# Kernel optimization log

Measured on AMD Instinct MI355X. Metric: run time of the kernel, lower is better.

## Reference

```python
import jax, jax.numpy as jnp
import numpy as np


def setup_inputs() -> dict:
    key = jax.random.key(0)
    k1, k2, k3, k4 = jax.random.split(key, 4)
    B, T, C, H = 256, 320, 1024, 64
    x = jax.random.normal(k1, (B, T, C), dtype=jnp.float32)
    # nn.Linear weights stored as (in, out) for x @ W
    scale = 1.0 / np.sqrt(C)
    W_key = jax.random.normal(k2, (C, H), dtype=jnp.float32) * scale
    W_query = jax.random.normal(k3, (C, H), dtype=jnp.float32) * scale
    W_value = jax.random.normal(k4, (C, H), dtype=jnp.float32) * scale
    return {"x": x, "W_key": W_key, "W_query": W_query, "W_value": W_value}


def reference(x, W_key, W_query, W_value):
    # Single-head causal self-attention. Dropout is identity (eval mode).
    B, T, C = x.shape
    k = x @ W_key     # [B,T,H]
    q = x @ W_query   # [B,T,H]
    v = x @ W_value   # [B,T,H]
    # NOTE: source scales by C**-0.5 with C = embd_size (input dim), not head_size.
    scale = jnp.asarray(C, x.dtype) ** -0.5
    wei = jnp.einsum("bth,bsh->bts", q, k) * scale  # [B,T,T]
    causal = jnp.tril(jnp.ones((T, T), dtype=bool))
    wei = jnp.where(causal, wei, -jnp.inf)
    wei = jax.nn.softmax(wei, axis=-1)
    out = jnp.einsum("bts,bsh->bth", wei, v)  # [B,T,H]
    return out
```

## Files before the change

kernel.cpp:

```cpp
#include <hip/hip_runtime.h>

typedef __bf16 bf16;
typedef __bf16 bf16x4 __attribute__((ext_vector_type(4)));
typedef __bf16 bf16x8 __attribute__((ext_vector_type(8)));
typedef float f32x4 __attribute__((ext_vector_type(4)));

#define MFMA16(a, b, c) __builtin_amdgcn_mfma_f32_16x16x32_bf16((a), (b), (c), 0, 0, 0)

#define GLD16(gp, lp)                                                              \
  __builtin_amdgcn_global_load_lds(                                                \
      (const __attribute__((address_space(1))) unsigned int*)(unsigned long long)(gp), \
      (__attribute__((address_space(3))) unsigned int*)(unsigned long long)(lp), 16, 0, 0)


__global__ __launch_bounds__(256) void wtrans_kernel(
    const float* __restrict__ Wk, const float* __restrict__ Wq,
    const float* __restrict__ Wv, bf16* __restrict__ Wt) {
  __shared__ bf16 tile[64][65];
  const int mat = blockIdx.x >> 4;
  const int kt = (blockIdx.x & 15) << 6;
  const float* __restrict__ W = (mat == 0) ? Wk : ((mat == 1) ? Wq : Wv);
  const int tid = threadIdx.x;
#pragma unroll
  for (int j = 0; j < 16; ++j) {
    const int i = tid + 256 * j;
    const int k = i >> 6, h = i & 63;
    tile[h][k] = (bf16)W[(kt + k) * 64 + h];
  }
  __syncthreads();
#pragma unroll
  for (int j = 0; j < 16; ++j) {
    const int i = tid + 256 * j;
    const int h = i >> 6, k = i & 63;
    Wt[mat * 65536 + h * 1024 + kt + k] = tile[h][k];
  }
}

__global__ __launch_bounds__(256) void qkv_kernel(
    const float* __restrict__ x, const bf16* __restrict__ Wt,
    bf16* __restrict__ Qw, bf16* __restrict__ Kw, bf16* __restrict__ Vt) {
  __shared__ float xs3[3][64][64];
  const int tid = threadIdx.x;
  const int w = tid >> 6, l = tid & 63;
  const int lr = l & 15, lg = l >> 4;
  const int m0 = blockIdx.x * 64;

  f32x4 acc[4][3];
#pragma unroll
  for (int mf = 0; mf < 4; ++mf)
#pragma unroll
    for (int nf = 0; nf < 3; ++nf) acc[mf][nf] = (f32x4)0.0f;

  const char* gb0;
  const char* gb1;
  const char* gb2;
  const char* gb3;
  {
    const int rr = l >> 4;
    const int cb = (l & 15) * 16;
    gb0 = (const char*)(x + (size_t)(m0 + 16 * w + 0 + rr) * 1024) + (cb ^ (((0 + rr) & 7) << 4));
    gb1 = (const char*)(x + (size_t)(m0 + 16 * w + 4 + rr) * 1024) + (cb ^ (((4 + rr) & 7) << 4));
    gb2 = (const char*)(x + (size_t)(m0 + 16 * w + 8 + rr) * 1024) + (cb ^ (((0 + rr) & 7) << 4));
    gb3 = (const char*)(x + (size_t)(m0 + 16 * w + 12 + rr) * 1024) + (cb ^ (((4 + rr) & 7) << 4));
  }

  bf16x8 wf[3][2];
  auto loadw = [&](int kt) {
#pragma unroll
    for (int nf = 0; nf < 3; ++nf) {
      const int colg = w * 48 + nf * 16 + lr;
      const bf16* p = Wt + (colg >> 6) * 65536 + (colg & 63) * 1024 + kt + lg * 8;
      wf[nf][0] = *(const bf16x8*)p;
      wf[nf][1] = *(const bf16x8*)(p + 32);
    }
  };
  auto dma = [&](int t) {
    char* lb = (char*)&xs3[t % 3][16 * w][0];
    const int ko = t * 256;
    GLD16(gb0 + ko, lb + 0 * 1024);
    GLD16(gb1 + ko, lb + 1 * 1024);
    GLD16(gb2 + ko, lb + 2 * 1024);
    GLD16(gb3 + ko, lb + 3 * 1024);
  };

  dma(0);
  dma(1);
  const int sw = (lr & 7) << 4;
#pragma unroll
  for (int t = 0; t < 16; ++t) {
    if (t < 15) {
      asm volatile("s_waitcnt vmcnt(4)" ::: "memory");
    } else {
      asm volatile("s_waitcnt vmcnt(0)" ::: "memory");
    }
    __builtin_amdgcn_sched_barrier(0);
    __builtin_amdgcn_s_barrier();
    __builtin_amdgcn_sched_barrier(0);
    loadw(t * 64);
    if (t < 14) dma(t + 2);
    const char* xb = (const char*)&xs3[t % 3][0][0];
#pragma unroll
    for (int mf = 0; mf < 4; ++mf) {
      const char* rp = xb + (mf * 16 + lr) * 256;
      const f32x4 f0 = *(const f32x4*)(rp + ((lg * 32 + 0) ^ sw));
      const f32x4 f1 = *(const f32x4*)(rp + ((lg * 32 + 16) ^ sw));
      const f32x4 f2 = *(const f32x4*)(rp + (128 + ((lg * 32 + 0) ^ sw)));
      const f32x4 f3 = *(const f32x4*)(rp + (128 + ((lg * 32 + 16) ^ sw)));
      bf16x8 a0, a1;
#pragma unroll
      for (int j = 0; j < 4; ++j) {
        a0[j] = (bf16)f0[j]; a0[4 + j] = (bf16)f1[j];
        a1[j] = (bf16)f2[j]; a1[4 + j] = (bf16)f3[j];
      }
#pragma unroll
      for (int nf = 0; nf < 3; ++nf) {
        acc[mf][nf] = MFMA16(a0, wf[nf][0], acc[mf][nf]);
        acc[mf][nf] = MFMA16(a1, wf[nf][1], acc[mf][nf]);
      }
    }
  }

#pragma unroll
  for (int mf = 0; mf < 4; ++mf) {
#pragma unroll
    for (int nf = 0; nf < 3; ++nf) {
      const int colg = w * 48 + nf * 16 + lr;
      const int mat = colg >> 6, h = colg & 63;
      const int mb = m0 + mf * 16 + lg * 4;
      if (mat == 2) {
        const int b = mb / 320, t = mb % 320;
        bf16x4 o;
#pragma unroll
        for (int r = 0; r < 4; ++r) o[r] = (bf16)acc[mf][nf][r];
        *(bf16x4*)(Vt + ((size_t)b * 64 + h) * 320 + t) = o;
      } else {
        bf16* __restrict__ dst = (mat == 0) ? Kw : Qw;
#pragma unroll
        for (int r = 0; r < 4; ++r) dst[(size_t)(mb + r) * 64 + h] = (bf16)acc[mf][nf][r];
      }
    }
  }
}

template <int QT>
__device__ __forceinline__ void attn_impl(
    int b, const bf16* __restrict__ Qw, const bf16* __restrict__ Kw,
    const bf16* __restrict__ Vt, float* __restrict__ out,
    char* Ks, char* Vs, char* Ps) {
  constexpr int NT = QT + 1;
  const int tid = threadIdx.x;
  const int w = tid >> 6, l = tid & 63;
  const int lr = l & 15, lg = l >> 4;
  const int t0 = QT * 64 + w * 16;
  const int tq = t0 + lr;

  const bf16* qp = Qw + ((size_t)b * 320 + tq) * 64 + lg * 8;
  const bf16x8 bq0 = *(const bf16x8*)qp;
  const bf16x8 bq1 = *(const bf16x8*)(qp + 32);

  f32x4 acc[NT * 4];
#pragma unroll
  for (int i = 0; i < NT * 4; ++i) acc[i] = (f32x4)0.0f;

  bf16x8 kg0, kg1;
  const int krow = w * 16 + (l >> 2);
  const int kcb = (l & 3) * 16;
  const int ksw = (krow & 7) << 4;
  auto gloadK = [&](int st) {
    const bf16* src = Kw + ((size_t)b * 320 + st * 64 + krow) * 64 + (l & 3) * 8;
    kg0 = *(const bf16x8*)src;
    kg1 = *(const bf16x8*)(src + 32);
  };
  auto dswriteK = [&](int buf) {
    char* base = Ks + buf * 8192 + krow * 128;
    *(bf16x8*)(base + (kcb ^ ksw)) = kg0;
    *(bf16x8*)(base + ((kcb + 64) ^ ksw)) = kg1;
  };

  gloadK(0);
  dswriteK(0);
  asm volatile("s_waitcnt lgkmcnt(0)" ::: "memory");
  __builtin_amdgcn_s_barrier();

  const int asw = (lr & 7) << 4;
#pragma unroll
  for (int st = 0; st < NT; ++st) {
    if (st < QT) gloadK(st + 1);
    const char* kb = Ks + (st & 1) * 8192;
#pragma unroll
    for (int nf = 0; nf < 4; ++nf) {
      const char* rp = kb + (nf * 16 + lr) * 128;
      const bf16x8 a0 = *(const bf16x8*)(rp + ((lg * 16) ^ asw));
      const bf16x8 a1 = *(const bf16x8*)(rp + ((64 + lg * 16) ^ asw));
      acc[st * 4 + nf] = MFMA16(a0, bq0, acc[st * 4 + nf]);
      acc[st * 4 + nf] = MFMA16(a1, bq1, acc[st * 4 + nf]);
    }
    if (st < QT) {
      dswriteK((st + 1) & 1);
      asm volatile("s_waitcnt lgkmcnt(0)" ::: "memory");
      __builtin_amdgcn_s_barrier();
    }
  }

  uint2 vg[4];
  const int vrow = w * 16 + (l >> 4);
  auto gloadV = [&](int st) {
    const bf16* src = Vt + ((size_t)b * 64 + vrow) * 320 + st * 64 + (l & 15) * 4;
#pragma unroll
    for (int i = 0; i < 4; ++i) vg[i] = *(const uint2*)(src + i * 4 * 320);
  };
  auto dswriteV = [&](int buf) {
#pragma unroll
    for (int i = 0; i < 4; ++i) {
      const int hl = vrow + i * 4;
      *(uint2*)(Vs + buf * 8192 + hl * 128 + (((l & 15) * 8) ^ ((hl & 7) << 4))) = vg[i];
    }
  };
  gloadV(0);

  float mx = -1e30f;
#pragma unroll
  for (int st = 0; st < NT; ++st)
#pragma unroll
    for (int nf = 0; nf < 4; ++nf)
#pragma unroll
      for (int r = 0; r < 4; ++r) {
        const int sg = st * 64 + nf * 16 + lg * 4 + r;
        float v = acc[st * 4 + nf][r] * 0.03125f;
        v = (sg > tq) ? -1e30f : v;
        acc[st * 4 + nf][r] = v;
        mx = fmaxf(mx, v);
      }
  mx = fmaxf(mx, __shfl_xor(mx, 16));
  mx = fmaxf(mx, __shfl_xor(mx, 32));
  float sum = 0.f;
#pragma unroll
  for (int i = 0; i < NT * 4; ++i)
#pragma unroll
    for (int r = 0; r < 4; ++r) {
      const float p = __expf(acc[i][r] - mx);
      acc[i][r] = p;
      sum += p;
    }
  sum += __shfl_xor(sum, 16);
  sum += __shfl_xor(sum, 32);
  const float rinv = 1.0f / sum;

  dswriteV(0);
  asm volatile("s_waitcnt lgkmcnt(0)" ::: "memory");
  __builtin_amdgcn_s_barrier();

  char* Pw = Ps + w * 2048;
  f32x4 ao[4];
#pragma unroll
  for (int hf = 0; hf < 4; ++hf) ao[hf] = (f32x4)0.0f;

#pragma unroll
  for (int st = 0; st < NT; ++st) {
    if (st < QT) gloadV(st + 1);
#pragma unroll
    for (int nf = 0; nf < 4; ++nf) {
      bf16x4 o;
#pragma unroll
      for (int r = 0; r < 4; ++r) o[r] = (bf16)(acc[st * 4 + nf][r] * rinv);
      *(bf16x4*)(Pw + lr * 128 + ((nf * 32 + lg * 8) ^ asw)) = o;
    }
    const char* vb = Vs + (st & 1) * 8192;
#pragma unroll
    for (int ks = 0; ks < 2; ++ks) {
      const bf16x8 ap = *(const bf16x8*)(Pw + lr * 128 + ((ks * 64 + lg * 16) ^ asw));
#pragma unroll
      for (int hf = 0; hf < 4; ++hf) {
        const bf16x8 bv =
            *(const bf16x8*)(vb + (hf * 16 + lr) * 128 + ((ks * 64 + lg * 16) ^ asw));
        ao[hf] = MFMA16(ap, bv, ao[hf]);
      }
    }
    if (st < QT) {
      dswriteV((st + 1) & 1);
      asm volatile("s_waitcnt lgkmcnt(0)" ::: "memory");
      __builtin_amdgcn_s_barrier();
    }
  }

  const int rowb = t0 + lg * 4;
#pragma unroll
  for (int hf = 0; hf < 4; ++hf)
#pragma unroll
    for (int r = 0; r < 4; ++r)
      out[((size_t)b * 320 + rowb + r) * 64 + hf * 16 + lr] = ao[hf][r];
}

__global__ __launch_bounds__(256) void attn_kernel(
    const bf16* __restrict__ Qw, const bf16* __restrict__ Kw,
    const bf16* __restrict__ Vt, float* __restrict__ out) {
  __shared__ __align__(16) char Ks[2 * 8192];
  __shared__ __align__(16) char Vs[2 * 8192];
  __shared__ __align__(16) char Ps[4 * 2048];
  const int b = blockIdx.x;
  const int qt = 4 - blockIdx.y;
  switch (qt) {
    case 0: attn_impl<0>(b, Qw, Kw, Vt, out, Ks, Vs, Ps); break;
    case 1: attn_impl<1>(b, Qw, Kw, Vt, out, Ks, Vs, Ps); break;
    case 2: attn_impl<2>(b, Qw, Kw, Vt, out, Ks, Vs, Ps); break;
    case 3: attn_impl<3>(b, Qw, Kw, Vt, out, Ks, Vs, Ps); break;
    default: attn_impl<4>(b, Qw, Kw, Vt, out, Ks, Vs, Ps); break;
  }
}

extern "C" void kernel_launch(void* const* d_in, const int* in_sizes, int n_in,
                              void* d_out, int out_size, void* d_ws, size_t ws_size,
                              hipStream_t stream) {
  const float* x  = (const float*)d_in[0];
  const float* Wk = (const float*)d_in[1];
  const float* Wq = (const float*)d_in[2];
  const float* Wv = (const float*)d_in[3];
  float* out = (float*)d_out;

  bf16* Wt = (bf16*)d_ws;
  bf16* Qw = Wt + 3 * 64 * 1024;
  bf16* Kw = Qw + (size_t)81920 * 64;
  bf16* Vt = Kw + (size_t)81920 * 64;

  hipLaunchKernelGGL(wtrans_kernel, dim3(48), dim3(256), 0, stream, Wk, Wq, Wv, Wt);
  hipLaunchKernelGGL(qkv_kernel, dim3(1280), dim3(256), 0, stream, x, Wt, Qw, Kw, Vt);
  hipLaunchKernelGGL(attn_kernel, dim3(256, 5), dim3(256), 0, stream, Qw, Kw, Vt, out);
}
```

Before: 119.1 us.

## Prefetch all K and V tiles into registers up front in attention

Issues global loads for every K tile at kernel start and all V tiles during the QK loop, holding them in registers. The LDS writes for the next tile then happen before the current compute instead of after it, so global latency is no longer exposed once per tile. Sched barriers around the s_barrier keep the compiler from moving instructions across the sync. This raises register pressure considerably (up to 5 tiles of K and V per thread), which may reduce occupancy or cause spills.

```diff
diff --git a/kernel.cpp b/kernel.cpp
--- a/kernel.cpp
+++ b/kernel.cpp
@@ -11,6 +11,14 @@
   __builtin_amdgcn_global_load_lds(                                                \
       (const __attribute__((address_space(1))) unsigned int*)(unsigned long long)(gp), \
       (__attribute__((address_space(3))) unsigned int*)(unsigned long long)(lp), 16, 0, 0)
+
+#define LGKM0_BARRIER()                                   \
+  do {                                                    \
+    asm volatile("s_waitcnt lgkmcnt(0)" ::: "memory");    \
+    __builtin_amdgcn_sched_barrier(0);                    \
+    __builtin_amdgcn_s_barrier();                         \
+    __builtin_amdgcn_sched_barrier(0);                    \
+  } while (0)
 
 
 __global__ __launch_bounds__(256) void wtrans_kernel(
@@ -158,34 +166,44 @@
   const bf16x8 bq0 = *(const bf16x8*)qp;
   const bf16x8 bq1 = *(const bf16x8*)(qp + 32);
 
-  f32x4 acc[NT * 4];
-#pragma unroll
-  for (int i = 0; i < NT * 4; ++i) acc[i] = (f32x4)0.0f;
-
-  bf16x8 kg0, kg1;
   const int krow = w * 16 + (l >> 2);
   const int kcb = (l & 3) * 16;
   const int ksw = (krow & 7) << 4;
-  auto gloadK = [&](int st) {
-    const bf16* src = Kw + ((size_t)b * 320 + st * 64 + krow) * 64 + (l & 3) * 8;
-    kg0 = *(const bf16x8*)src;
-    kg1 = *(const bf16x8*)(src + 32);
-  };
-  auto dswriteK = [&](int buf) {
-    char* base = Ks + buf * 8192 + krow * 128;
-    *(bf16x8*)(base + (kcb ^ ksw)) = kg0;
-    *(bf16x8*)(base + ((kcb + 64) ^ ksw)) = kg1;
-  };
-
-  gloadK(0);
-  dswriteK(0);
-  asm volatile("s_waitcnt lgkmcnt(0)" ::: "memory");
-  __builtin_amdgcn_s_barrier();
+  const bf16* kbase = Kw + ((size_t)b * 320 + krow) * 64 + (l & 3) * 8;
+  bf16x8 kr0[NT], kr1[NT];
+#pragma unroll
+  for (int st = 0; st < NT; ++st) {
+    kr0[st] = *(const bf16x8*)(kbase + st * 4096);
+    kr1[st] = *(const bf16x8*)(kbase + st * 4096 + 32);
+  }
+
+  const int vrow = w * 16 + (l >> 4);
+  const bf16* vbase = Vt + ((size_t)b * 64 + vrow) * 320 + (l & 15) * 4;
+  uint2 vr[NT][4];
+
+  f32x4 acc[NT * 4];
+#pragma unroll
+  for (int i = 0; i < NT * 4; ++i) acc[i] = (f32x4)0.0f;
+
+  {
+    char* base = Ks + 0 * 8192 + krow * 128;
+    *(bf16x8*)(base + (kcb ^ ksw)) = kr0[0];
+    *(bf16x8*)(base + ((kcb + 64) ^ ksw)) = kr1[0];
+  }
+  LGKM0_BARRIER();
 
   const int asw = (lr & 7) << 4;
 #pragma unroll
   for (int st = 0; st < NT; ++st) {
-    if (st < QT) gloadK(st + 1);
+    if (st + 1 < NT) {
+      char* base = Ks + ((st + 1) & 1) * 8192 + krow * 128;
+      *(bf16x8*)(base + (kcb ^ ksw)) = kr0[st + 1];
+      *(bf16x8*)(base + ((kcb + 64) ^ ksw)) = kr1[st + 1];
+    }
+#pragma unroll
+    for (int i = 0; i < 4; ++i)
+      vr[st][i] = *(const uint2*)(vbase + i * 1280 + st * 64);
+
     const char* kb = Ks + (st & 1) * 8192;
 #pragma unroll
     for (int nf = 0; nf < 4; ++nf) {
@@ -195,28 +213,16 @@
       acc[st * 4 + nf] = MFMA16(a0, bq0, acc[st * 4 + nf]);
       acc[st * 4 + nf] = MFMA16(a1, bq1, acc[st * 4 + nf]);
     }
-    if (st < QT) {
-      dswriteK((st + 1) & 1);
-      asm volatile("s_waitcnt lgkmcnt(0)" ::: "memory");
-      __builtin_amdgcn_s_barrier();
-    }
-  }
-
-  uint2 vg[4];
-  const int vrow = w * 16 + (l >> 4);
-  auto gloadV = [&](int st) {
-    const bf16* src = Vt + ((size_t)b * 64 + vrow) * 320 + st * 64 + (l & 15) * 4;
-#pragma unroll
-    for (int i = 0; i < 4; ++i) vg[i] = *(const uint2*)(src + i * 4 * 320);
-  };
-  auto dswriteV = [&](int buf) {
+    if (st + 1 < NT) LGKM0_BARRIER();
+  }
+
+  {
 #pragma unroll
     for (int i = 0; i < 4; ++i) {
       const int hl = vrow + i * 4;
-      *(uint2*)(Vs + buf * 8192 + hl * 128 + (((l & 15) * 8) ^ ((hl & 7) << 4))) = vg[i];
-    }
-  };
-  gloadV(0);
+      *(uint2*)(Vs + 0 * 8192 + hl * 128 + (((l & 15) * 8) ^ ((hl & 7) << 4))) = vr[0][i];
+    }
+  }
 
   float mx = -1e30f;
 #pragma unroll
@@ -246,9 +252,7 @@
   sum += __shfl_xor(sum, 32);
   const float rinv = 1.0f / sum;
 
-  dswriteV(0);
-  asm volatile("s_waitcnt lgkmcnt(0)" ::: "memory");
-  __builtin_amdgcn_s_barrier();
+  LGKM0_BARRIER();
 
   char* Pw = Ps + w * 2048;
   f32x4 ao[4];
@@ -257,7 +261,14 @@
 
 #pragma unroll
   for (int st = 0; st < NT; ++st) {
-    if (st < QT) gloadV(st + 1);
+    if (st + 1 < NT) {
+#pragma unroll
+      for (int i = 0; i < 4; ++i) {
+        const int hl = vrow + i * 4;
+        *(uint2*)(Vs + ((st + 1) & 1) * 8192 + hl * 128 +
+                  (((l & 15) * 8) ^ ((hl & 7) << 4))) = vr[st + 1][i];
+      }
+    }
 #pragma unroll
     for (int nf = 0; nf < 4; ++nf) {
       bf16x4 o;
@@ -276,11 +287,7 @@
         ao[hf] = MFMA16(ap, bv, ao[hf]);
       }
     }
-    if (st < QT) {
-      dswriteV((st + 1) & 1);
-      asm volatile("s_waitcnt lgkmcnt(0)" ::: "memory");
-      __builtin_amdgcn_s_barrier();
-    }
+    if (st + 1 < NT) LGKM0_BARRIER();
   }
 
   const int rowb = t0 + lg * 4;
```

Result: no change. 120.6 us (+1.2%).

## Stage weights in LDS and stream x directly into registers in QKV projection

Applied to the files above, without the earlier changes.

The QKV projection is restructured. Weight tiles are now DMA'd into double-buffered LDS, while each wave loads its 16 rows of x straight from global memory into registers, double-buffered across steps. Each wave computes all 192 output columns for its rows, instead of the previous split of 64 rows by 48 columns per wave. This drops the LDS round trip for the large fp32 activation stream and reuses the shared weights across waves. In exchange it relies on the memory system to hide x load latency without LDS staging, and it uses more accumulator registers.

```diff
diff --git a/kernel.cpp b/kernel.cpp
--- a/kernel.cpp
+++ b/kernel.cpp
@@ -39,55 +39,47 @@
 __global__ __launch_bounds__(256) void qkv_kernel(
     const float* __restrict__ x, const bf16* __restrict__ Wt,
     bf16* __restrict__ Qw, bf16* __restrict__ Kw, bf16* __restrict__ Vt) {
-  __shared__ float xs3[3][64][64];
+  __shared__ __align__(16) bf16 Ws[2][192 * 64];
   const int tid = threadIdx.x;
   const int w = tid >> 6, l = tid & 63;
   const int lr = l & 15, lg = l >> 4;
   const int m0 = blockIdx.x * 64;
-
-  f32x4 acc[4][3];
-#pragma unroll
-  for (int mf = 0; mf < 4; ++mf)
-#pragma unroll
-    for (int nf = 0; nf < 3; ++nf) acc[mf][nf] = (f32x4)0.0f;
-
-  const char* gb0;
-  const char* gb1;
-  const char* gb2;
-  const char* gb3;
-  {
-    const int rr = l >> 4;
-    const int cb = (l & 15) * 16;
-    gb0 = (const char*)(x + (size_t)(m0 + 16 * w + 0 + rr) * 1024) + (cb ^ (((0 + rr) & 7) << 4));
-    gb1 = (const char*)(x + (size_t)(m0 + 16 * w + 4 + rr) * 1024) + (cb ^ (((4 + rr) & 7) << 4));
-    gb2 = (const char*)(x + (size_t)(m0 + 16 * w + 8 + rr) * 1024) + (cb ^ (((0 + rr) & 7) << 4));
-    gb3 = (const char*)(x + (size_t)(m0 + 16 * w + 12 + rr) * 1024) + (cb ^ (((4 + rr) & 7) << 4));
-  }
-
-  bf16x8 wf[3][2];
-  auto loadw = [&](int kt) {
-#pragma unroll
-    for (int nf = 0; nf < 3; ++nf) {
-      const int colg = w * 48 + nf * 16 + lr;
-      const bf16* p = Wt + (colg >> 6) * 65536 + (colg & 63) * 1024 + kt + lg * 8;
-      wf[nf][0] = *(const bf16x8*)p;
-      wf[nf][1] = *(const bf16x8*)(p + 32);
-    }
-  };
-  auto dma = [&](int t) {
-    char* lb = (char*)&xs3[t % 3][16 * w][0];
-    const int ko = t * 256;
-    GLD16(gb0 + ko, lb + 0 * 1024);
-    GLD16(gb1 + ko, lb + 1 * 1024);
-    GLD16(gb2 + ko, lb + 2 * 1024);
-    GLD16(gb3 + ko, lb + 3 * 1024);
-  };
-
-  dma(0);
-  dma(1);
+  const int r0 = m0 + 16 * w;
+
+  f32x4 acc[12];
+#pragma unroll
+  for (int nf = 0; nf < 12; ++nf) acc[nf] = (f32x4)0.0f;
+
+  const char* wsrc[6];
+#pragma unroll
+  for (int j = 0; j < 6; ++j) {
+    const int g = 48 * w + 8 * j + (l >> 3);
+    wsrc[j] = (const char*)(Wt + (g >> 6) * 65536 + (g & 63) * 1024) +
+              (((l & 7) * 16) ^ ((g & 7) << 4));
+  }
+  auto wdma = [&](int t) {
+    char* lb = (char*)&Ws[t & 1][0];
+#pragma unroll
+    for (int j = 0; j < 6; ++j)
+      GLD16(wsrc[j] + t * 128, lb + (48 * w + 8 * j) * 128);
+  };
+
+  const char* xsrc = (const char*)(x + (size_t)(r0 + lr) * 1024) + lg * 32;
+  f32x4 gA[4], gB[4];
+  auto xload = [&](int t, f32x4* g) {
+    const char* p = xsrc + t * 256;
+    g[0] = *(const f32x4*)(p);
+    g[1] = *(const f32x4*)(p + 16);
+    g[2] = *(const f32x4*)(p + 128);
+    g[3] = *(const f32x4*)(p + 144);
+  };
+
+  wdma(0);
+  xload(0, gA);
+  xload(1, gB);
+
   const int sw = (lr & 7) << 4;
-#pragma unroll
-  for (int t = 0; t < 16; ++t) {
+  auto step = [&](int t, f32x4* g) {
     if (t < 15) {
       asm volatile("s_waitcnt vmcnt(4)" ::: "memory");
     } else {
@@ -96,48 +88,48 @@
     __builtin_amdgcn_sched_barrier(0);
     __builtin_amdgcn_s_barrier();
     __builtin_amdgcn_sched_barrier(0);
-    loadw(t * 64);
-    if (t < 14) dma(t + 2);
-    const char* xb = (const char*)&xs3[t % 3][0][0];
-#pragma unroll
-    for (int mf = 0; mf < 4; ++mf) {
-      const char* rp = xb + (mf * 16 + lr) * 256;
-      const f32x4 f0 = *(const f32x4*)(rp + ((lg * 32 + 0) ^ sw));
-      const f32x4 f1 = *(const f32x4*)(rp + ((lg * 32 + 16) ^ sw));
-      const f32x4 f2 = *(const f32x4*)(rp + (128 + ((lg * 32 + 0) ^ sw)));
-      const f32x4 f3 = *(const f32x4*)(rp + (128 + ((lg * 32 + 16) ^ sw)));
-      bf16x8 a0, a1;
-#pragma unroll
-      for (int j = 0; j < 4; ++j) {
-        a0[j] = (bf16)f0[j]; a0[4 + j] = (bf16)f1[j];
-        a1[j] = (bf16)f2[j]; a1[4 + j] = (bf16)f3[j];
-      }
-#pragma unroll
-      for (int nf = 0; nf < 3; ++nf) {
-        acc[mf][nf] = MFMA16(a0, wf[nf][0], acc[mf][nf]);
-        acc[mf][nf] = MFMA16(a1, wf[nf][1], acc[mf][nf]);
-      }
-    }
-  }
-
-#pragma unroll
-  for (int mf = 0; mf < 4; ++mf) {
-#pragma unroll
-    for (int nf = 0; nf < 3; ++nf) {
-      const int colg = w * 48 + nf * 16 + lr;
-      const int mat = colg >> 6, h = colg & 63;
-      const int mb = m0 + mf * 16 + lg * 4;
-      if (mat == 2) {
-        const int b = mb / 320, t = mb % 320;
-        bf16x4 o;
-#pragma unroll
-        for (int r = 0; r < 4; ++r) o[r] = (bf16)acc[mf][nf][r];
-        *(bf16x4*)(Vt + ((size_t)b * 64 + h) * 320 + t) = o;
-      } else {
-        bf16* __restrict__ dst = (mat == 0) ? Kw : Qw;
-#pragma unroll
-        for (int r = 0; r < 4; ++r) dst[(size_t)(mb + r) * 64 + h] = (bf16)acc[mf][nf][r];
-      }
+
+    bf16x8 a0, a1;
+#pragma unroll
+    for (int i = 0; i < 4; ++i) {
+      a0[i] = (bf16)g[0][i]; a0[4 + i] = (bf16)g[1][i];
+      a1[i] = (bf16)g[2][i]; a1[4 + i] = (bf16)g[3][i];
+    }
+    if (t < 15) wdma(t + 1);
+    if (t < 14) xload(t + 2, g);
+
+    const char* wb = (const char*)&Ws[t & 1][0];
+#pragma unroll
+    for (int nf = 0; nf < 12; ++nf) {
+      const char* rp = wb + (nf * 16 + lr) * 128;
+      const bf16x8 b0 = *(const bf16x8*)(rp + ((lg * 16) ^ sw));
+      const bf16x8 b1 = *(const bf16x8*)(rp + ((64 + lg * 16) ^ sw));
+      acc[nf] = MFMA16(a0, b0, acc[nf]);
+      acc[nf] = MFMA16(a1, b1, acc[nf]);
+    }
+  };
+
+#pragma unroll
+  for (int t2 = 0; t2 < 16; t2 += 2) {
+    step(t2, gA);
+    step(t2 + 1, gB);
+  }
+
+#pragma unroll
+  for (int nf = 0; nf < 12; ++nf) {
+    const int mat = nf >> 2;
+    const int h = (nf & 3) * 16 + lr;
+    const int mb = r0 + lg * 4;
+    if (mat == 2) {
+      const int bb = mb / 320, tt = mb % 320;
+      bf16x4 o;
+#pragma unroll
+      for (int r = 0; r < 4; ++r) o[r] = (bf16)acc[nf][r];
+      *(bf16x4*)(Vt + ((size_t)bb * 64 + h) * 320 + tt) = o;
+    } else {
+      bf16* __restrict__ dst = (mat == 0) ? Kw : Qw;
+#pragma unroll
+      for (int r = 0; r < 4; ++r) dst[(size_t)(mb + r) * 64 + h] = (bf16)acc[nf][r];
     }
   }
 }
```

New measurement: 115.8 us. 1.03x faster.
